# Kernel tuning notes

Measured on AMD Instinct MI355X. Metric: run time of the kernel, lower is better.

Reference implementation:

```python
import jax, jax.numpy as jnp
import numpy as np

B, T, H, L = 64, 256, 512, 2

def setup_inputs() -> dict:
    key = jax.random.key(0)
    ks = jax.random.split(key, 5)
    s = 0.05  # keep gate pre-activations in a sane range
    return {
        "x": jax.random.normal(ks[0], (B, T, H), jnp.float32),
        "Wi": jax.random.normal(ks[1], (L, H, 4 * H), jnp.float32) * s,
        "Wh": jax.random.normal(ks[2], (L, H, 4 * H), jnp.float32) * s,
        "bi": jax.random.normal(ks[3], (L, 4 * H), jnp.float32) * s,
        "bh": jax.random.normal(ks[4], (L, 4 * H), jnp.float32) * s,
    }

def _lstm(x, Wi, Wh, bi, bh):
    b, t, _ = x.shape
    L_, H_ = Wi.shape[0], Wi.shape[2] // 4
    h0 = jnp.zeros((L_, b, H_), x.dtype)
    c0 = jnp.zeros((L_, b, H_), x.dtype)

    def step(carry, x_t):
        h, c = carry
        hs, cs = [], []
        inp = x_t  # [B, H]
        for l in range(L_):
            gates = inp @ Wi[l] + bi[l] + h[l] @ Wh[l] + bh[l]  # [B, 4H]
            i, f, g, o = jnp.split(gates, 4, axis=-1)
            i, f, o = jax.nn.sigmoid(i), jax.nn.sigmoid(f), jax.nn.sigmoid(o)
            g = jnp.tanh(g)
            new_c = f * c[l] + i * g
            new_h = o * jnp.tanh(new_c)
            hs.append(new_h)
            cs.append(new_c)
            inp = new_h
        return (jnp.stack(hs), jnp.stack(cs)), inp

    (hT, cT), outs = jax.lax.scan(step, (h0, c0), jnp.swapaxes(x, 0, 1))
    return jnp.swapaxes(outs, 0, 1), (hT, cT)  # [B,T,H], ([L,B,H],[L,B,H])

def reference(x, Wi, Wh, bi, bh):
    return _lstm(x, Wi, Wh, bi, bh)
```

## Files before the change

kernel.cpp:

```cpp
#include <hip/hip_runtime.h>

typedef __attribute__((ext_vector_type(8))) short short8;
typedef __attribute__((ext_vector_type(4))) float f32x4;
typedef __attribute__((ext_vector_type(4))) float fvec4;
typedef __attribute__((ext_vector_type(4))) unsigned short u16x4;

#define B_ 64
#define T_ 256
#define H_ 512
#define NG 2048
#define BTH (64*256*512)
#define BH (64*512)
#define FPAD 64

__device__ __forceinline__ float bf2f(unsigned short u) {
    return __builtin_bit_cast(float, ((unsigned)u) << 16);
}
__device__ __forceinline__ unsigned short f2bf(float f) {
    unsigned u = __builtin_bit_cast(unsigned, f);
    u += 0x7fffu + ((u >> 16) & 1u);
    return (unsigned short)(u >> 16);
}
__device__ __forceinline__ float sigm(float x) { return 1.f / (1.f + __expf(-x)); }
__device__ __forceinline__ float tanh_f(float x) {
    x = fminf(15.f, fmaxf(-15.f, x));
    float e = __expf(-2.f * x);
    return (1.f - e) / (1.f + e);
}

__device__ __forceinline__ void store_coh(unsigned* p, unsigned v) {
    __hip_atomic_store(p, v, __ATOMIC_RELAXED, __HIP_MEMORY_SCOPE_AGENT);
}
__device__ __forceinline__ void drain_vm() {
    asm volatile("s_waitcnt vmcnt(0)" ::: "memory");
}
__device__ __forceinline__ void wv_wait(const unsigned* fl, int w, unsigned target) {
    const unsigned* p = fl + (size_t)(((threadIdx.x & 31) << 2) + w) * FPAD;
    int spins = 0;
    for (;;) {
        unsigned v = __hip_atomic_load(p, __ATOMIC_RELAXED, __HIP_MEMORY_SCOPE_AGENT);
        if (__all((int)(v >= target))) break;
        __builtin_amdgcn_s_sleep(1);
        if (++spins > 400000) break;
    }
    asm volatile("" ::: "memory");
}

__global__ void transpose_cvt(const float* __restrict__ Wi, const float* __restrict__ Wh,
                              unsigned short* __restrict__ Wt) {
    __shared__ float tile[64][65];
    int z = blockIdx.z;
    const float* src = (z < 2 ? Wi : Wh) + (size_t)(z & 1) * H_ * NG;
    unsigned short* dst = Wt + (size_t)z * NG * H_;
    int k0 = blockIdx.x * 64, n0 = blockIdx.y * 64;
    int tx = threadIdx.x & 63, ty = threadIdx.x >> 6;
#pragma unroll
    for (int p = 0; p < 16; ++p) {
        int r = (p << 2) + ty;
        tile[r][tx] = src[(size_t)(k0 + r) * NG + n0 + tx];
    }
    __syncthreads();
#pragma unroll
    for (int p = 0; p < 16; ++p) {
        int r = (p << 2) + ty;
        dst[(size_t)(n0 + r) * H_ + k0 + tx] = f2bf(tile[tx][r]);
    }
}

__global__ void cvt_bf16(const float* __restrict__ x, unsigned short* __restrict__ xb) {
    size_t i = ((size_t)blockIdx.x * 256 + threadIdx.x) * 4;
    fvec4 v = *(const fvec4*)&x[i];
    u16x4 o;
    o[0] = f2bf(v[0]); o[1] = f2bf(v[1]); o[2] = f2bf(v[2]); o[3] = f2bf(v[3]);
    *(u16x4*)&xb[i] = o;
}

__global__ __launch_bounds__(256) void gemm_bt(
    const unsigned short* __restrict__ A, const unsigned short* __restrict__ Bt,
    const float* __restrict__ bias1, const float* __restrict__ bias2,
    unsigned short* __restrict__ C) {
    const int tid = threadIdx.x;
    const int wave = tid >> 6, lane = tid & 63;
    const int quad = lane >> 4, l15 = lane & 15;
    const int row0 = blockIdx.x * 64 + wave * 16;
    const int col0 = blockIdx.y * 64;
    f32x4 acc[4] = {};
    const unsigned short* ap = A + (size_t)(row0 + l15) * H_ + (quad << 3);
    const unsigned short* bp = Bt + (size_t)(col0 + l15) * H_ + (quad << 3);
#pragma unroll
    for (int kk = 0; kk < H_; kk += 32) {
        short8 a = *(const short8*)(ap + kk);
#pragma unroll
        for (int c4 = 0; c4 < 4; ++c4) {
            short8 b = *(const short8*)(bp + (size_t)(c4 << 4) * H_ + kk);
            acc[c4] = __builtin_amdgcn_mfma_f32_16x16x32_bf16(a, b, acc[c4], 0, 0, 0);
        }
    }
#pragma unroll
    for (int c4 = 0; c4 < 4; ++c4) {
        int col = col0 + (c4 << 4) + l15;
        float bs = bias1[col] + bias2[col];
        int g = col >> 9;
        int blk = (col & 511) >> 4;
#pragma unroll
        for (int r = 0; r < 4; ++r) {
            int row = row0 + (quad << 2) + r;
            int t = row & 255, b = row >> 8;
            C[((size_t)blk << 20) + ((size_t)t << 12) + (g << 10) + (b << 4) + l15] =
                f2bf(acc[c4][r] + bs);
        }
    }
}

__global__ __launch_bounds__(256, 1) void lstm_fused(
    const unsigned short* __restrict__ Gi,
    const unsigned short* __restrict__ Wt,
    unsigned* __restrict__ h0h,
    unsigned* __restrict__ h1h,
    const float* __restrict__ bi, const float* __restrict__ bh,
    float* __restrict__ out,
    float* __restrict__ hT, float* __restrict__ cT,
    unsigned* __restrict__ flags) {
    __shared__ unsigned short wi_lds[64 * 512];
    const size_t NK = (size_t)NG * H_;
    const int tid = threadIdx.x;
    const int wave = tid >> 6, lane = tid & 63;
    const int quad = lane >> 4, l15 = lane & 15;
    const int m0 = wave << 4;
    unsigned* flag0 = flags;
    unsigned* flag1 = flags + 128 * FPAD;
    const size_t hoff = ((size_t)(quad >> 1) << 9) + ((size_t)(m0 + l15) << 3) + ((quad & 1) << 2);

    if (blockIdx.x < 32) {
        const int slot = (int)blockIdx.x;
        const int j0 = slot << 4;
        const unsigned short* Wht = Wt + 2 * NK;
        short8 bw[64];
#pragma unroll
        for (int kb = 0; kb < 16; ++kb)
#pragma unroll
            for (int g = 0; g < 4; ++g)
                bw[kb * 4 + g] =
                    *(const short8*)&Wht[(size_t)((g << 9) + j0 + l15) * H_ + (kb << 5) + (quad << 3)];
#pragma unroll
        for (int i = 0; i < 64; ++i) asm volatile("" : "+v"(bw[i]));

        if (!(l15 & 1)) {
            unsigned* hz = h0h + ((size_t)(slot * 64) << 3) + (l15 >> 1);
#pragma unroll
            for (int r = 0; r < 4; ++r)
                store_coh(&hz[(size_t)(m0 + (quad << 2) + r) << 3], 0u);
        }
        float cc[4] = {0.f, 0.f, 0.f, 0.f};
        drain_vm();
        store_coh(&flag0[(size_t)((slot << 2) + wave) * FPAD], 1u);

        float gv[4][4];
#pragma unroll
        for (int r = 0; r < 4; ++r) {
            int b = m0 + (quad << 2) + r;
#pragma unroll
            for (int g = 0; g < 4; ++g)
                gv[g][r] = bf2f(Gi[((size_t)slot << 20) + (g << 10) + (b << 4) + l15]);
        }

        for (int t = 0; t < T_; ++t) {
            wv_wait(flag0, wave, (unsigned)(t + 1));
            const unsigned* ap = h0h + ((size_t)t << 14) + hoff;
            short8 ha[16];
#pragma unroll
            for (int kb = 0; kb < 16; ++kb) ha[kb] = *(const short8*)(ap + (kb << 10));

            f32x4 acc0 = {}, acc1 = {}, acc2 = {}, acc3 = {};
#pragma unroll
            for (int kb = 0; kb < 16; ++kb) {
                acc0 = __builtin_amdgcn_mfma_f32_16x16x32_bf16(ha[kb], bw[kb * 4 + 0], acc0, 0, 0, 0);
                acc1 = __builtin_amdgcn_mfma_f32_16x16x32_bf16(ha[kb], bw[kb * 4 + 1], acc1, 0, 0, 0);
                acc2 = __builtin_amdgcn_mfma_f32_16x16x32_bf16(ha[kb], bw[kb * 4 + 2], acc2, 0, 0, 0);
                acc3 = __builtin_amdgcn_mfma_f32_16x16x32_bf16(ha[kb], bw[kb * 4 + 3], acc3, 0, 0, 0);
            }

            unsigned* hw = h0h + ((size_t)(t + 1) << 14) + ((size_t)(slot * 64) << 3) + (l15 >> 1);
            float hvv[4];
#pragma unroll
            for (int r = 0; r < 4; ++r) {
                float iv = sigm(acc0[r] + gv[0][r]);
                float fv = sigm(acc1[r] + gv[1][r]);
                float gg = tanh_f(acc2[r] + gv[2][r]);
                float ov = sigm(acc3[r] + gv[3][r]);
                float cn = fv * cc[r] + iv * gg;
                cc[r] = cn;
                float hv = ov * tanh_f(cn);
                hvv[r] = hv;
                unsigned short hb16 = f2bf(hv);
                unsigned packed = (unsigned)hb16 |
                                  (((unsigned)(unsigned short)__shfl_xor((int)hb16, 1)) << 16);
                if (!(l15 & 1))
                    store_coh(&hw[(size_t)(m0 + (quad << 2) + r) << 3], packed);
            }
            if (t == T_ - 1) {
#pragma unroll
                for (int r = 0; r < 4; ++r) {
                    int b = m0 + (quad << 2) + r;
                    int jj = j0 + l15;
                    hT[((size_t)b << 9) + jj] = hvv[r];
                    cT[((size_t)b << 9) + jj] = cc[r];
                }
            }
            drain_vm();
            store_coh(&flag0[(size_t)((slot << 2) + wave) * FPAD], (unsigned)(t + 2));

            int tn = (t + 1) & (T_ - 1);
#pragma unroll
            for (int r = 0; r < 4; ++r) {
                int b = m0 + (quad << 2) + r;
#pragma unroll
                for (int g = 0; g < 4; ++g)
                    gv[g][r] = bf2f(Gi[((size_t)slot << 20) + ((size_t)tn << 12) +
                                       (g << 10) + (b << 4) + l15]);
            }
        }
    } else {
        const int slot = (int)blockIdx.x - 32;
        const int j0 = slot << 4;
        const unsigned short* Wht = Wt + 3 * NK;
        short8 bw[64];
#pragma unroll
        for (int kb = 0; kb < 16; ++kb)
#pragma unroll
            for (int g = 0; g < 4; ++g)
                bw[kb * 4 + g] =
                    *(const short8*)&Wht[(size_t)((g << 9) + j0 + l15) * H_ + (kb << 5) + (quad << 3)];
#pragma unroll
        for (int i = 0; i < 64; ++i) asm volatile("" : "+v"(bw[i]));

        const unsigned short* Wit = Wt + 1 * NK;
#pragma unroll
        for (int i2 = 0; i2 < 16; ++i2) {
            int c = i2 * 256 + tid;
            int l = c & 15, q = (c >> 4) & 3, g = (c >> 6) & 3, kb = c >> 8;
            short8 v = *(const short8*)&Wit[(size_t)((g << 9) + j0 + l) * H_ + (kb << 5) + (q << 3)];
            *(short8*)((char*)wi_lds + ((size_t)c << 4)) = v;
        }
        __syncthreads();
        const int wbase = (quad << 8) + (l15 << 4);

        float gb0 = bi[NG + j0 + l15]        + bh[NG + j0 + l15];
        float gb1 = bi[NG + 512 + j0 + l15]  + bh[NG + 512 + j0 + l15];
        float gb2 = bi[NG + 1024 + j0 + l15] + bh[NG + 1024 + j0 + l15];
        float gb3 = bi[NG + 1536 + j0 + l15] + bh[NG + 1536 + j0 + l15];

        if (!(l15 & 1)) {
            unsigned* hz = h1h + ((size_t)(slot * 64) << 3) + (l15 >> 1);
#pragma unroll
            for (int r = 0; r < 4; ++r)
                store_coh(&hz[(size_t)(m0 + (quad << 2) + r) << 3], 0u);
        }
        float cc[4] = {0.f, 0.f, 0.f, 0.f};
        drain_vm();
        store_coh(&flag1[(size_t)((slot << 2) + wave) * FPAD], 1u);

        short8 ha1[16], ha0[16];
        wv_wait(flag1, wave, 1u);
        {
            const unsigned* ap1 = h1h + hoff;
#pragma unroll
            for (int kb = 0; kb < 16; ++kb) ha1[kb] = *(const short8*)(ap1 + (kb << 10));
        }
        wv_wait(flag0, wave, 2u);
        {
            const unsigned* ap0 = h0h + ((size_t)1 << 14) + hoff;
#pragma unroll
            for (int kb = 0; kb < 16; ++kb) ha0[kb] = *(const short8*)(ap0 + (kb << 10));
        }

        for (int t = 0; t < T_; ++t) {
            f32x4 acc0 = {}, acc1 = {}, acc2 = {}, acc3 = {};
#pragma unroll
            for (int kb = 0; kb < 16; ++kb) {
                acc0 = __builtin_amdgcn_mfma_f32_16x16x32_bf16(ha1[kb], bw[kb * 4 + 0], acc0, 0, 0, 0);
                acc1 = __builtin_amdgcn_mfma_f32_16x16x32_bf16(ha1[kb], bw[kb * 4 + 1], acc1, 0, 0, 0);
                acc2 = __builtin_amdgcn_mfma_f32_16x16x32_bf16(ha1[kb], bw[kb * 4 + 2], acc2, 0, 0, 0);
                acc3 = __builtin_amdgcn_mfma_f32_16x16x32_bf16(ha1[kb], bw[kb * 4 + 3], acc3, 0, 0, 0);
            }
#pragma unroll
            for (int kb = 0; kb < 16; ++kb) {
                const char* base = (const char*)wi_lds + (kb << 12) + wbase;
                short8 w0 = *(const short8*)(base);
                short8 w1 = *(const short8*)(base + (1 << 10));
                short8 w2 = *(const short8*)(base + (2 << 10));
                short8 w3 = *(const short8*)(base + (3 << 10));
                acc0 = __builtin_amdgcn_mfma_f32_16x16x32_bf16(ha0[kb], w0, acc0, 0, 0, 0);
                acc1 = __builtin_amdgcn_mfma_f32_16x16x32_bf16(ha0[kb], w1, acc1, 0, 0, 0);
                acc2 = __builtin_amdgcn_mfma_f32_16x16x32_bf16(ha0[kb], w2, acc2, 0, 0, 0);
                acc3 = __builtin_amdgcn_mfma_f32_16x16x32_bf16(ha0[kb], w3, acc3, 0, 0, 0);
            }

            unsigned* hw = h1h + ((size_t)(t + 1) << 14) + ((size_t)(slot * 64) << 3) + (l15 >> 1);
            float hvv[4];
#pragma unroll
            for (int r = 0; r < 4; ++r) {
                float iv = sigm(acc0[r] + gb0);
                float fv = sigm(acc1[r] + gb1);
                float gg = tanh_f(acc2[r] + gb2);
                float ov = sigm(acc3[r] + gb3);
                float cn = fv * cc[r] + iv * gg;
                cc[r] = cn;
                float hv = ov * tanh_f(cn);
                hvv[r] = hv;
                unsigned short hb16 = f2bf(hv);
                unsigned packed = (unsigned)hb16 |
                                  (((unsigned)(unsigned short)__shfl_xor((int)hb16, 1)) << 16);
                if (!(l15 & 1))
                    store_coh(&hw[(size_t)(m0 + (quad << 2) + r) << 3], packed);
            }
#pragma unroll
            for (int r = 0; r < 4; ++r) {
                int b = m0 + (quad << 2) + r;
                int jj = j0 + l15;
                out[((size_t)((b << 8) + t)) * H_ + jj] = hvv[r];
            }
            if (t == T_ - 1) {
#pragma unroll
                for (int r = 0; r < 4; ++r) {
                    int b = m0 + (quad << 2) + r;
                    int jj = j0 + l15;
                    hT[BH + ((size_t)b << 9) + jj] = hvv[r];
                    cT[BH + ((size_t)b << 9) + jj] = cc[r];
                }
                break;
            }
            drain_vm();
            store_coh(&flag1[(size_t)((slot << 2) + wave) * FPAD], (unsigned)(t + 2));

            wv_wait(flag0, wave, (unsigned)(t + 3));
            const unsigned* ap0 = h0h + ((size_t)(t + 2) << 14) + hoff;
#pragma unroll
            for (int kb = 0; kb < 16; ++kb) ha0[kb] = *(const short8*)(ap0 + (kb << 10));
            wv_wait(flag1, wave, (unsigned)(t + 2));
            const unsigned* ap1 = h1h + ((size_t)(t + 1) << 14) + hoff;
#pragma unroll
            for (int kb = 0; kb < 16; ++kb) ha1[kb] = *(const short8*)(ap1 + (kb << 10));
        }
    }
}

extern "C" void kernel_launch(void* const* d_in, const int* in_sizes, int n_in,
                              void* d_out, int out_size, void* d_ws, size_t ws_size,
                              hipStream_t stream) {
    const float* x  = (const float*)d_in[0];
    const float* Wi = (const float*)d_in[1];
    const float* Wh = (const float*)d_in[2];
    const float* bi = (const float*)d_in[3];
    const float* bh = (const float*)d_in[4];
    float* out = (float*)d_out;

    char* w = (char*)d_ws;
    const size_t NK = (size_t)NG * H_;
    unsigned short* Wt  = (unsigned short*)w;
    unsigned short* xb  = Wt + 4 * NK;
    unsigned short* Gi  = xb + (size_t)16384 * H_;
    unsigned* h0h       = (unsigned*)(Gi + (size_t)16384 * NG);
    unsigned* h1h       = h0h + (size_t)(T_ + 1) * 16384;
    unsigned* flags     = h1h + (size_t)(T_ + 1) * 16384;

    hipMemsetAsync(flags, 0, 2 * 128 * FPAD * sizeof(unsigned), stream);

    transpose_cvt<<<dim3(8, 32, 4), 256, 0, stream>>>(Wi, Wh, Wt);
    cvt_bf16<<<8192, 256, 0, stream>>>(x, xb);

    gemm_bt<<<dim3(256, 32), 256, 0, stream>>>(xb, Wt + 0 * NK, bi, bh, Gi);

    lstm_fused<<<64, 256, 0, stream>>>(Gi, Wt, h0h, h1h, bi, bh,
                                       out, out + BTH, out + BTH + 2 * (size_t)BH, flags);
}
```

Before: 2.137 ms.

## Fuse layer-0 input projection into recurrent kernel and merge layer-1 flag waits

Removes the separate input-projection GEMM and its Gi buffer. Layer-0 blocks now compute x_t·Wi on the fly from LDS-resident Wi, using an x layout transposed to time-major, and prefetch the next timestep's x after publishing h. Layer-1 blocks use one combined spin-wait on both layer flags per step instead of two sequential waits, and no longer prefetch across iterations. This saves the GEMM launch and its memory traffic, but adds MFMA and LDS work to layer 0's serial critical path.

After: 2.966 ms. +38.8%, slower.

```diff
diff --git a/kernel.cpp b/kernel.cpp
--- a/kernel.cpp
+++ b/kernel.cpp
@@ -45,6 +45,21 @@
     }
     asm volatile("" ::: "memory");
 }
+__device__ __forceinline__ void wv_wait2(const unsigned* fA, unsigned tA,
+                                         const unsigned* fB, unsigned tB, int w) {
+    const int l = threadIdx.x & 63;
+    const unsigned* p = (l < 32) ? fA + (size_t)(((l & 31) << 2) + w) * FPAD
+                                 : fB + (size_t)(((l & 31) << 2) + w) * FPAD;
+    const unsigned tgt = (l < 32) ? tA : tB;
+    int spins = 0;
+    for (;;) {
+        unsigned v = __hip_atomic_load(p, __ATOMIC_RELAXED, __HIP_MEMORY_SCOPE_AGENT);
+        if (__all((int)(v >= tgt))) break;
+        __builtin_amdgcn_s_sleep(1);
+        if (++spins > 400000) break;
+    }
+    asm volatile("" ::: "memory");
+}
 
 __global__ void transpose_cvt(const float* __restrict__ Wi, const float* __restrict__ Wh,
                               unsigned short* __restrict__ Wt) {
@@ -67,53 +82,19 @@
     }
 }
 
-__global__ void cvt_bf16(const float* __restrict__ x, unsigned short* __restrict__ xb) {
+__global__ void cvt_blk(const float* __restrict__ x, unsigned short* __restrict__ xb) {
     size_t i = ((size_t)blockIdx.x * 256 + threadIdx.x) * 4;
+    int h = (int)(i & 511);
+    size_t r2 = i >> 9;
+    int t = (int)(r2 & 255), b = (int)(r2 >> 8);
     fvec4 v = *(const fvec4*)&x[i];
     u16x4 o;
     o[0] = f2bf(v[0]); o[1] = f2bf(v[1]); o[2] = f2bf(v[2]); o[3] = f2bf(v[3]);
-    *(u16x4*)&xb[i] = o;
-}
-
-__global__ __launch_bounds__(256) void gemm_bt(
-    const unsigned short* __restrict__ A, const unsigned short* __restrict__ Bt,
-    const float* __restrict__ bias1, const float* __restrict__ bias2,
-    unsigned short* __restrict__ C) {
-    const int tid = threadIdx.x;
-    const int wave = tid >> 6, lane = tid & 63;
-    const int quad = lane >> 4, l15 = lane & 15;
-    const int row0 = blockIdx.x * 64 + wave * 16;
-    const int col0 = blockIdx.y * 64;
-    f32x4 acc[4] = {};
-    const unsigned short* ap = A + (size_t)(row0 + l15) * H_ + (quad << 3);
-    const unsigned short* bp = Bt + (size_t)(col0 + l15) * H_ + (quad << 3);
-#pragma unroll
-    for (int kk = 0; kk < H_; kk += 32) {
-        short8 a = *(const short8*)(ap + kk);
-#pragma unroll
-        for (int c4 = 0; c4 < 4; ++c4) {
-            short8 b = *(const short8*)(bp + (size_t)(c4 << 4) * H_ + kk);
-            acc[c4] = __builtin_amdgcn_mfma_f32_16x16x32_bf16(a, b, acc[c4], 0, 0, 0);
-        }
-    }
-#pragma unroll
-    for (int c4 = 0; c4 < 4; ++c4) {
-        int col = col0 + (c4 << 4) + l15;
-        float bs = bias1[col] + bias2[col];
-        int g = col >> 9;
-        int blk = (col & 511) >> 4;
-#pragma unroll
-        for (int r = 0; r < 4; ++r) {
-            int row = row0 + (quad << 2) + r;
-            int t = row & 255, b = row >> 8;
-            C[((size_t)blk << 20) + ((size_t)t << 12) + (g << 10) + (b << 4) + l15] =
-                f2bf(acc[c4][r] + bs);
-        }
-    }
+    *(u16x4*)&xb[(((size_t)t << 6) + b) * H_ + h] = o;
 }
 
 __global__ __launch_bounds__(256, 1) void lstm_fused(
-    const unsigned short* __restrict__ Gi,
+    const unsigned short* __restrict__ xb,
     const unsigned short* __restrict__ Wt,
     unsigned* __restrict__ h0h,
     unsigned* __restrict__ h1h,
@@ -130,38 +111,55 @@
     unsigned* flag0 = flags;
     unsigned* flag1 = flags + 128 * FPAD;
     const size_t hoff = ((size_t)(quad >> 1) << 9) + ((size_t)(m0 + l15) << 3) + ((quad & 1) << 2);
-
-    if (blockIdx.x < 32) {
-        const int slot = (int)blockIdx.x;
-        const int j0 = slot << 4;
-        const unsigned short* Wht = Wt + 2 * NK;
-        short8 bw[64];
-#pragma unroll
-        for (int kb = 0; kb < 16; ++kb)
-#pragma unroll
-            for (int g = 0; g < 4; ++g)
-                bw[kb * 4 + g] =
-                    *(const short8*)&Wht[(size_t)((g << 9) + j0 + l15) * H_ + (kb << 5) + (quad << 3)];
-#pragma unroll
-        for (int i = 0; i < 64; ++i) asm volatile("" : "+v"(bw[i]));
-
+    const int wbase = (quad << 8) + (l15 << 4);
+    const int is_l1 = (blockIdx.x >= 32);
+    const int slot = (int)blockIdx.x & 31;
+    const int j0 = slot << 4;
+
+    const unsigned short* Wht = Wt + (is_l1 ? 3 : 2) * NK;
+    short8 bw[64];
+#pragma unroll
+    for (int kb = 0; kb < 16; ++kb)
+#pragma unroll
+        for (int g = 0; g < 4; ++g)
+            bw[kb * 4 + g] =
+                *(const short8*)&Wht[(size_t)((g << 9) + j0 + l15) * H_ + (kb << 5) + (quad << 3)];
+#pragma unroll
+    for (int i = 0; i < 64; ++i) asm volatile("" : "+v"(bw[i]));
+
+    const unsigned short* Wit = Wt + (is_l1 ? 1 : 0) * NK;
+#pragma unroll
+    for (int i2 = 0; i2 < 16; ++i2) {
+        int c = i2 * 256 + tid;
+        int l = c & 15, q = (c >> 4) & 3, g = (c >> 6) & 3, kb = c >> 8;
+        short8 v = *(const short8*)&Wit[(size_t)((g << 9) + j0 + l) * H_ + (kb << 5) + (q << 3)];
+        *(short8*)((char*)wi_lds + ((size_t)c << 4)) = v;
+    }
+    __syncthreads();
+
+    const int boff = is_l1 ? NG : 0;
+    float gb0 = bi[boff + j0 + l15]        + bh[boff + j0 + l15];
+    float gb1 = bi[boff + 512 + j0 + l15]  + bh[boff + 512 + j0 + l15];
+    float gb2 = bi[boff + 1024 + j0 + l15] + bh[boff + 1024 + j0 + l15];
+    float gb3 = bi[boff + 1536 + j0 + l15] + bh[boff + 1536 + j0 + l15];
+
+    float cc[4] = {0.f, 0.f, 0.f, 0.f};
+
+    if (!is_l1) {
         if (!(l15 & 1)) {
             unsigned* hz = h0h + ((size_t)(slot * 64) << 3) + (l15 >> 1);
 #pragma unroll
             for (int r = 0; r < 4; ++r)
                 store_coh(&hz[(size_t)(m0 + (quad << 2) + r) << 3], 0u);
         }
-        float cc[4] = {0.f, 0.f, 0.f, 0.f};
         drain_vm();
         store_coh(&flag0[(size_t)((slot << 2) + wave) * FPAD], 1u);
 
-        float gv[4][4];
-#pragma unroll
-        for (int r = 0; r < 4; ++r) {
-            int b = m0 + (quad << 2) + r;
-#pragma unroll
-            for (int g = 0; g < 4; ++g)
-                gv[g][r] = bf2f(Gi[((size_t)slot << 20) + (g << 10) + (b << 4) + l15]);
+        short8 xa[16];
+        {
+            const unsigned short* xp = xb + (size_t)(m0 + l15) * H_ + (quad << 3);
+#pragma unroll
+            for (int kb = 0; kb < 16; ++kb) xa[kb] = *(const short8*)(xp + (kb << 5));
         }
 
         for (int t = 0; t < T_; ++t) {
@@ -178,110 +176,6 @@
                 acc1 = __builtin_amdgcn_mfma_f32_16x16x32_bf16(ha[kb], bw[kb * 4 + 1], acc1, 0, 0, 0);
                 acc2 = __builtin_amdgcn_mfma_f32_16x16x32_bf16(ha[kb], bw[kb * 4 + 2], acc2, 0, 0, 0);
                 acc3 = __builtin_amdgcn_mfma_f32_16x16x32_bf16(ha[kb], bw[kb * 4 + 3], acc3, 0, 0, 0);
-            }
-
-            unsigned* hw = h0h + ((size_t)(t + 1) << 14) + ((size_t)(slot * 64) << 3) + (l15 >> 1);
-            float hvv[4];
-#pragma unroll
-            for (int r = 0; r < 4; ++r) {
-                float iv = sigm(acc0[r] + gv[0][r]);
-                float fv = sigm(acc1[r] + gv[1][r]);
-                float gg = tanh_f(acc2[r] + gv[2][r]);
-                float ov = sigm(acc3[r] + gv[3][r]);
-                float cn = fv * cc[r] + iv * gg;
-                cc[r] = cn;
-                float hv = ov * tanh_f(cn);
-                hvv[r] = hv;
-                unsigned short hb16 = f2bf(hv);
-                unsigned packed = (unsigned)hb16 |
-                                  (((unsigned)(unsigned short)__shfl_xor((int)hb16, 1)) << 16);
-                if (!(l15 & 1))
-                    store_coh(&hw[(size_t)(m0 + (quad << 2) + r) << 3], packed);
-            }
-            if (t == T_ - 1) {
-#pragma unroll
-                for (int r = 0; r < 4; ++r) {
-                    int b = m0 + (quad << 2) + r;
-                    int jj = j0 + l15;
-                    hT[((size_t)b << 9) + jj] = hvv[r];
-                    cT[((size_t)b << 9) + jj] = cc[r];
-                }
-            }
-            drain_vm();
-            store_coh(&flag0[(size_t)((slot << 2) + wave) * FPAD], (unsigned)(t + 2));
-
-            int tn = (t + 1) & (T_ - 1);
-#pragma unroll
-            for (int r = 0; r < 4; ++r) {
-                int b = m0 + (quad << 2) + r;
-#pragma unroll
-                for (int g = 0; g < 4; ++g)
-                    gv[g][r] = bf2f(Gi[((size_t)slot << 20) + ((size_t)tn << 12) +
-                                       (g << 10) + (b << 4) + l15]);
-            }
-        }
-    } else {
-        const int slot = (int)blockIdx.x - 32;
-        const int j0 = slot << 4;
-        const unsigned short* Wht = Wt + 3 * NK;
-        short8 bw[64];
-#pragma unroll
-        for (int kb = 0; kb < 16; ++kb)
-#pragma unroll
-            for (int g = 0; g < 4; ++g)
-                bw[kb * 4 + g] =
-                    *(const short8*)&Wht[(size_t)((g << 9) + j0 + l15) * H_ + (kb << 5) + (quad << 3)];
-#pragma unroll
-        for (int i = 0; i < 64; ++i) asm volatile("" : "+v"(bw[i]));
-
-        const unsigned short* Wit = Wt + 1 * NK;
-#pragma unroll
-        for (int i2 = 0; i2 < 16; ++i2) {
-            int c = i2 * 256 + tid;
-            int l = c & 15, q = (c >> 4) & 3, g = (c >> 6) & 3, kb = c >> 8;
-            short8 v = *(const short8*)&Wit[(size_t)((g << 9) + j0 + l) * H_ + (kb << 5) + (q << 3)];
-            *(short8*)((char*)wi_lds + ((size_t)c << 4)) = v;
-        }
-        __syncthreads();
-        const int wbase = (quad << 8) + (l15 << 4);
-
-        float gb0 = bi[NG + j0 + l15]        + bh[NG + j0 + l15];
-        float gb1 = bi[NG + 512 + j0 + l15]  + bh[NG + 512 + j0 + l15];
-        float gb2 = bi[NG + 1024 + j0 + l15] + bh[NG + 1024 + j0 + l15];
-        float gb3 = bi[NG + 1536 + j0 + l15] + bh[NG + 1536 + j0 + l15];
-
-        if (!(l15 & 1)) {
-            unsigned* hz = h1h + ((size_t)(slot * 64) << 3) + (l15 >> 1);
-#pragma unroll
-            for (int r = 0; r < 4; ++r)
-                store_coh(&hz[(size_t)(m0 + (quad << 2) + r) << 3], 0u);
-        }
-        float cc[4] = {0.f, 0.f, 0.f, 0.f};
-        drain_vm();
-        store_coh(&flag1[(size_t)((slot << 2) + wave) * FPAD], 1u);
-
-        short8 ha1[16], ha0[16];
-        wv_wait(flag1, wave, 1u);
-        {
-            const unsigned* ap1 = h1h + hoff;
-#pragma unroll
-            for (int kb = 0; kb < 16; ++kb) ha1[kb] = *(const short8*)(ap1 + (kb << 10));
-        }
-        wv_wait(flag0, wave, 2u);
-        {
-            const unsigned* ap0 = h0h + ((size_t)1 << 14) + hoff;
-#pragma unroll
-            for (int kb = 0; kb < 16; ++kb) ha0[kb] = *(const short8*)(ap0 + (kb << 10));
-        }
-
-        for (int t = 0; t < T_; ++t) {
-            f32x4 acc0 = {}, acc1 = {}, acc2 = {}, acc3 = {};
-#pragma unroll
-            for (int kb = 0; kb < 16; ++kb) {
-                acc0 = __builtin_amdgcn_mfma_f32_16x16x32_bf16(ha1[kb], bw[kb * 4 + 0], acc0, 0, 0, 0);
-                acc1 = __builtin_amdgcn_mfma_f32_16x16x32_bf16(ha1[kb], bw[kb * 4 + 1], acc1, 0, 0, 0);
-                acc2 = __builtin_amdgcn_mfma_f32_16x16x32_bf16(ha1[kb], bw[kb * 4 + 2], acc2, 0, 0, 0);
-                acc3 = __builtin_amdgcn_mfma_f32_16x16x32_bf16(ha1[kb], bw[kb * 4 + 3], acc3, 0, 0, 0);
             }
 #pragma unroll
             for (int kb = 0; kb < 16; ++kb) {
@@ -290,13 +184,13 @@
                 short8 w1 = *(const short8*)(base + (1 << 10));
                 short8 w2 = *(const short8*)(base + (2 << 10));
                 short8 w3 = *(const short8*)(base + (3 << 10));
-                acc0 = __builtin_amdgcn_mfma_f32_16x16x32_bf16(ha0[kb], w0, acc0, 0, 0, 0);
-                acc1 = __builtin_amdgcn_mfma_f32_16x16x32_bf16(ha0[kb], w1, acc1, 0, 0, 0);
-                acc2 = __builtin_amdgcn_mfma_f32_16x16x32_bf16(ha0[kb], w2, acc2, 0, 0, 0);
-                acc3 = __builtin_amdgcn_mfma_f32_16x16x32_bf16(ha0[kb], w3, acc3, 0, 0, 0);
-            }
-
-            unsigned* hw = h1h + ((size_t)(t + 1) << 14) + ((size_t)(slot * 64) << 3) + (l15 >> 1);
+                acc0 = __builtin_amdgcn_mfma_f32_16x16x32_bf16(xa[kb], w0, acc0, 0, 0, 0);
+                acc1 = __builtin_amdgcn_mfma_f32_16x16x32_bf16(xa[kb], w1, acc1, 0, 0, 0);
+                acc2 = __builtin_amdgcn_mfma_f32_16x16x32_bf16(xa[kb], w2, acc2, 0, 0, 0);
+                acc3 = __builtin_amdgcn_mfma_f32_16x16x32_bf16(xa[kb], w3, acc3, 0, 0, 0);
+            }
+
+            unsigned* hw = h0h + ((size_t)(t + 1) << 14) + ((size_t)(slot * 64) << 3) + (l15 >> 1);
             float hvv[4];
 #pragma unroll
             for (int r = 0; r < 4; ++r) {
@@ -314,6 +208,86 @@
                 if (!(l15 & 1))
                     store_coh(&hw[(size_t)(m0 + (quad << 2) + r) << 3], packed);
             }
+            drain_vm();
+            store_coh(&flag0[(size_t)((slot << 2) + wave) * FPAD], (unsigned)(t + 2));
+
+            if (t < T_ - 1) {
+                const unsigned short* xp =
+                    xb + (((size_t)(t + 1) << 6) + (m0 + l15)) * H_ + (quad << 3);
+#pragma unroll
+                for (int kb = 0; kb < 16; ++kb) xa[kb] = *(const short8*)(xp + (kb << 5));
+            } else {
+#pragma unroll
+                for (int r = 0; r < 4; ++r) {
+                    int b = m0 + (quad << 2) + r;
+                    int jj = j0 + l15;
+                    hT[((size_t)b << 9) + jj] = hvv[r];
+                    cT[((size_t)b << 9) + jj] = cc[r];
+                }
+            }
+        }
+    } else {
+        if (!(l15 & 1)) {
+            unsigned* hz = h1h + ((size_t)(slot * 64) << 3) + (l15 >> 1);
+#pragma unroll
+            for (int r = 0; r < 4; ++r)
+                store_coh(&hz[(size_t)(m0 + (quad << 2) + r) << 3], 0u);
+        }
+        drain_vm();
+        store_coh(&flag1[(size_t)((slot << 2) + wave) * FPAD], 1u);
+
+        for (int t = 0; t < T_; ++t) {
+            wv_wait2(flag1, (unsigned)(t + 1), flag0, (unsigned)(t + 2), wave);
+            const unsigned* ap1 = h1h + ((size_t)t << 14) + hoff;
+            const unsigned* ap0 = h0h + ((size_t)(t + 1) << 14) + hoff;
+            short8 ha1[16], ha0[16];
+#pragma unroll
+            for (int kb = 0; kb < 16; ++kb) ha1[kb] = *(const short8*)(ap1 + (kb << 10));
+#pragma unroll
+            for (int kb = 0; kb < 16; ++kb) ha0[kb] = *(const short8*)(ap0 + (kb << 10));
+
+            f32x4 acc0 = {}, acc1 = {}, acc2 = {}, acc3 = {};
+#pragma unroll
+            for (int kb = 0; kb < 16; ++kb) {
+                acc0 = __builtin_amdgcn_mfma_f32_16x16x32_bf16(ha1[kb], bw[kb * 4 + 0], acc0, 0, 0, 0);
+                acc1 = __builtin_amdgcn_mfma_f32_16x16x32_bf16(ha1[kb], bw[kb * 4 + 1], acc1, 0, 0, 0);
+                acc2 = __builtin_amdgcn_mfma_f32_16x16x32_bf16(ha1[kb], bw[kb * 4 + 2], acc2, 0, 0, 0);
+                acc3 = __builtin_amdgcn_mfma_f32_16x16x32_bf16(ha1[kb], bw[kb * 4 + 3], acc3, 0, 0, 0);
+            }
+#pragma unroll
+            for (int kb = 0; kb < 16; ++kb) {
+                const char* base = (const char*)wi_lds + (kb << 12) + wbase;
+                short8 w0 = *(const short8*)(base);
+                short8 w1 = *(const short8*)(base + (1 << 10));
+                short8 w2 = *(const short8*)(base + (2 << 10));
+                short8 w3 = *(const short8*)(base + (3 << 10));
+                acc0 = __builtin_amdgcn_mfma_f32_16x16x32_bf16(ha0[kb], w0, acc0, 0, 0, 0);
+                acc1 = __builtin_amdgcn_mfma_f32_16x16x32_bf16(ha0[kb], w1, acc1, 0, 0, 0);
+                acc2 = __builtin_amdgcn_mfma_f32_16x16x32_bf16(ha0[kb], w2, acc2, 0, 0, 0);
+                acc3 = __builtin_amdgcn_mfma_f32_16x16x32_bf16(ha0[kb], w3, acc3, 0, 0, 0);
+            }
+
+            unsigned* hw = h1h + ((size_t)(t + 1) << 14) + ((size_t)(slot * 64) << 3) + (l15 >> 1);
+            float hvv[4];
+#pragma unroll
+            for (int r = 0; r < 4; ++r) {
+                float iv = sigm(acc0[r] + gb0);
+                float fv = sigm(acc1[r] + gb1);
+                float gg = tanh_f(acc2[r] + gb2);
+                float ov = sigm(acc3[r] + gb3);
+                float cn = fv * cc[r] + iv * gg;
+                cc[r] = cn;
+                float hv = ov * tanh_f(cn);
+                hvv[r] = hv;
+                unsigned short hb16 = f2bf(hv);
+                unsigned packed = (unsigned)hb16 |
+                                  (((unsigned)(unsigned short)__shfl_xor((int)hb16, 1)) << 16);
+                if (!(l15 & 1))
+                    store_coh(&hw[(size_t)(m0 + (quad << 2) + r) << 3], packed);
+            }
+            drain_vm();
+            store_coh(&flag1[(size_t)((slot << 2) + wave) * FPAD], (unsigned)(t + 2));
+
 #pragma unroll
             for (int r = 0; r < 4; ++r) {
                 int b = m0 + (quad << 2) + r;
@@ -328,19 +302,7 @@
                     hT[BH + ((size_t)b << 9) + jj] = hvv[r];
                     cT[BH + ((size_t)b << 9) + jj] = cc[r];
                 }
-                break;
-            }
-            drain_vm();
-            store_coh(&flag1[(size_t)((slot << 2) + wave) * FPAD], (unsigned)(t + 2));
-
-            wv_wait(flag0, wave, (unsigned)(t + 3));
-            const unsigned* ap0 = h0h + ((size_t)(t + 2) << 14) + hoff;
-#pragma unroll
-            for (int kb = 0; kb < 16; ++kb) ha0[kb] = *(const short8*)(ap0 + (kb << 10));
-            wv_wait(flag1, wave, (unsigned)(t + 2));
-            const unsigned* ap1 = h1h + ((size_t)(t + 1) << 14) + hoff;
-#pragma unroll
-            for (int kb = 0; kb < 16; ++kb) ha1[kb] = *(const short8*)(ap1 + (kb << 10));
+            }
         }
     }
 }
@@ -359,18 +321,15 @@
     const size_t NK = (size_t)NG * H_;
     unsigned short* Wt  = (unsigned short*)w;
     unsigned short* xb  = Wt + 4 * NK;
-    unsigned short* Gi  = xb + (size_t)16384 * H_;
-    unsigned* h0h       = (unsigned*)(Gi + (size_t)16384 * NG);
+    unsigned* h0h       = (unsigned*)(xb + (size_t)16384 * H_);
     unsigned* h1h       = h0h + (size_t)(T_ + 1) * 16384;
     unsigned* flags     = h1h + (size_t)(T_ + 1) * 16384;
 
     hipMemsetAsync(flags, 0, 2 * 128 * FPAD * sizeof(unsigned), stream);
 
     transpose_cvt<<<dim3(8, 32, 4), 256, 0, stream>>>(Wi, Wh, Wt);
-    cvt_bf16<<<8192, 256, 0, stream>>>(x, xb);
-
-    gemm_bt<<<dim3(256, 32), 256, 0, stream>>>(xb, Wt + 0 * NK, bi, bh, Gi);
-
-    lstm_fused<<<64, 256, 0, stream>>>(Gi, Wt, h0h, h1h, bi, bh,
+    cvt_blk<<<8192, 256, 0, stream>>>(x, xb);
+
+    lstm_fused<<<64, 256, 0, stream>>>(xb, Wt, h0h, h1h, bi, bh,
                                        out, out + BTH, out + BTH + 2 * (size_t)BH, flags);
 }
```

## Merge both LSTM layers into one block per slot with a single flag round

Applied to the files above, without the earlier changes.

Replaces the 64-block layout, where 32 blocks ran layer 0 and 32 ran layer 1 with separate flag arrays, with 32 blocks that each compute layer 0 at step rnd and layer 1 at step rnd-1 in the same round. Layer-1 recurrent weights stay in registers, while layer-0 recurrent weights and layer-1 input weights move to two LDS buffers. The aim is one cross-block barrier per round instead of two interleaved dependency chains, halving the number of flags to poll. In exchange each block does twice the MFMA work per step, reads Wh0 from LDS instead of registers, and runs on half as many CUs.

Result: slower. 2.466 ms (+15.4%).

```diff
diff --git a/kernel.cpp b/kernel.cpp
--- a/kernel.cpp
+++ b/kernel.cpp
@@ -121,226 +121,196 @@
     float* __restrict__ out,
     float* __restrict__ hT, float* __restrict__ cT,
     unsigned* __restrict__ flags) {
-    __shared__ unsigned short wi_lds[64 * 512];
+    __shared__ unsigned short w_lds[2][64 * 512];
     const size_t NK = (size_t)NG * H_;
     const int tid = threadIdx.x;
     const int wave = tid >> 6, lane = tid & 63;
     const int quad = lane >> 4, l15 = lane & 15;
     const int m0 = wave << 4;
-    unsigned* flag0 = flags;
-    unsigned* flag1 = flags + 128 * FPAD;
+    const int slot = (int)blockIdx.x;
+    const int j0 = slot << 4;
     const size_t hoff = ((size_t)(quad >> 1) << 9) + ((size_t)(m0 + l15) << 3) + ((quad & 1) << 2);
-
-    if (blockIdx.x < 32) {
-        const int slot = (int)blockIdx.x;
-        const int j0 = slot << 4;
-        const unsigned short* Wht = Wt + 2 * NK;
-        short8 bw[64];
-#pragma unroll
-        for (int kb = 0; kb < 16; ++kb)
-#pragma unroll
-            for (int g = 0; g < 4; ++g)
-                bw[kb * 4 + g] =
-                    *(const short8*)&Wht[(size_t)((g << 9) + j0 + l15) * H_ + (kb << 5) + (quad << 3)];
-#pragma unroll
-        for (int i = 0; i < 64; ++i) asm volatile("" : "+v"(bw[i]));
-
-        if (!(l15 & 1)) {
-            unsigned* hz = h0h + ((size_t)(slot * 64) << 3) + (l15 >> 1);
-#pragma unroll
-            for (int r = 0; r < 4; ++r)
-                store_coh(&hz[(size_t)(m0 + (quad << 2) + r) << 3], 0u);
-        }
-        float cc[4] = {0.f, 0.f, 0.f, 0.f};
-        drain_vm();
-        store_coh(&flag0[(size_t)((slot << 2) + wave) * FPAD], 1u);
-
-        float gv[4][4];
-#pragma unroll
-        for (int r = 0; r < 4; ++r) {
-            int b = m0 + (quad << 2) + r;
-#pragma unroll
-            for (int g = 0; g < 4; ++g)
-                gv[g][r] = bf2f(Gi[((size_t)slot << 20) + (g << 10) + (b << 4) + l15]);
-        }
-
-        for (int t = 0; t < T_; ++t) {
-            wv_wait(flag0, wave, (unsigned)(t + 1));
-            const unsigned* ap = h0h + ((size_t)t << 14) + hoff;
-            short8 ha[16];
-#pragma unroll
-            for (int kb = 0; kb < 16; ++kb) ha[kb] = *(const short8*)(ap + (kb << 10));
-
-            f32x4 acc0 = {}, acc1 = {}, acc2 = {}, acc3 = {};
+    const int wbase = (quad << 8) + (l15 << 4);
+
+    const unsigned short* Wh1t = Wt + 3 * NK;
+    short8 bw[64];
+#pragma unroll
+    for (int kb = 0; kb < 16; ++kb)
+#pragma unroll
+        for (int g = 0; g < 4; ++g)
+            bw[kb * 4 + g] =
+                *(const short8*)&Wh1t[(size_t)((g << 9) + j0 + l15) * H_ + (kb << 5) + (quad << 3)];
+#pragma unroll
+    for (int i = 0; i < 64; ++i) asm volatile("" : "+v"(bw[i]));
+
+    {
+        const unsigned short* srcs[2] = {Wt + 2 * NK, Wt + 1 * NK};
+#pragma unroll
+        for (int i2 = 0; i2 < 32; ++i2) {
+            int c = i2 * 256 + tid;
+            int sl = c >> 12, cc_ = c & 4095;
+            int l = cc_ & 15, q = (cc_ >> 4) & 3, g = (cc_ >> 6) & 3, kb = cc_ >> 8;
+            short8 v = *(const short8*)&srcs[sl][(size_t)((g << 9) + j0 + l) * H_ +
+                                                 (kb << 5) + (q << 3)];
+            *(short8*)((char*)&w_lds[sl][0] + ((size_t)cc_ << 4)) = v;
+        }
+    }
+
+    store_coh(&h0h[(size_t)slot * 512 + tid], 0u);
+    store_coh(&h0h[(size_t)slot * 512 + 256 + tid], 0u);
+    store_coh(&h1h[(size_t)slot * 512 + tid], 0u);
+    store_coh(&h1h[(size_t)slot * 512 + 256 + tid], 0u);
+    __syncthreads();
+    if (lane == 0) store_coh(&flags[(size_t)((slot << 2) + wave) * FPAD], 1u);
+
+    float gb0 = bi[NG + j0 + l15]        + bh[NG + j0 + l15];
+    float gb1 = bi[NG + 512 + j0 + l15]  + bh[NG + 512 + j0 + l15];
+    float gb2 = bi[NG + 1024 + j0 + l15] + bh[NG + 1024 + j0 + l15];
+    float gb3 = bi[NG + 1536 + j0 + l15] + bh[NG + 1536 + j0 + l15];
+
+    float gv[4][4];
+#pragma unroll
+    for (int r = 0; r < 4; ++r) {
+        int b = m0 + (quad << 2) + r;
+#pragma unroll
+        for (int g = 0; g < 4; ++g)
+            gv[g][r] = bf2f(Gi[((size_t)slot << 20) + (g << 10) + (b << 4) + l15]);
+    }
+
+    float cc0[4] = {0.f, 0.f, 0.f, 0.f};
+    float cc1[4] = {0.f, 0.f, 0.f, 0.f};
+
+    for (int rnd = 0; rnd <= T_; ++rnd) {
+        wv_wait(flags, wave, (unsigned)(rnd + 1));
+
+        const unsigned* ap0 = h0h + ((size_t)rnd << 14) + hoff;
+        short8 ha0[16];
+#pragma unroll
+        for (int kb = 0; kb < 16; ++kb) ha0[kb] = *(const short8*)(ap0 + (kb << 10));
+        short8 ha1[16];
+        if (rnd > 0) {
+            const unsigned* ap1 = h1h + ((size_t)(rnd - 1) << 14) + hoff;
+#pragma unroll
+            for (int kb = 0; kb < 16; ++kb) ha1[kb] = *(const short8*)(ap1 + (kb << 10));
+        }
+
+        if (rnd < T_) {
+            f32x4 a0 = {}, a1 = {}, a2 = {}, a3 = {};
 #pragma unroll
             for (int kb = 0; kb < 16; ++kb) {
-                acc0 = __builtin_amdgcn_mfma_f32_16x16x32_bf16(ha[kb], bw[kb * 4 + 0], acc0, 0, 0, 0);
-                acc1 = __builtin_amdgcn_mfma_f32_16x16x32_bf16(ha[kb], bw[kb * 4 + 1], acc1, 0, 0, 0);
-                acc2 = __builtin_amdgcn_mfma_f32_16x16x32_bf16(ha[kb], bw[kb * 4 + 2], acc2, 0, 0, 0);
-                acc3 = __builtin_amdgcn_mfma_f32_16x16x32_bf16(ha[kb], bw[kb * 4 + 3], acc3, 0, 0, 0);
-            }
-
-            unsigned* hw = h0h + ((size_t)(t + 1) << 14) + ((size_t)(slot * 64) << 3) + (l15 >> 1);
+                const char* base = (const char*)&w_lds[0][0] + (kb << 12) + wbase;
+                short8 w0 = *(const short8*)(base);
+                short8 w1 = *(const short8*)(base + (1 << 10));
+                short8 w2 = *(const short8*)(base + (2 << 10));
+                short8 w3 = *(const short8*)(base + (3 << 10));
+                a0 = __builtin_amdgcn_mfma_f32_16x16x32_bf16(ha0[kb], w0, a0, 0, 0, 0);
+                a1 = __builtin_amdgcn_mfma_f32_16x16x32_bf16(ha0[kb], w1, a1, 0, 0, 0);
+                a2 = __builtin_amdgcn_mfma_f32_16x16x32_bf16(ha0[kb], w2, a2, 0, 0, 0);
+                a3 = __builtin_amdgcn_mfma_f32_16x16x32_bf16(ha0[kb], w3, a3, 0, 0, 0);
+            }
+            unsigned* hw0 = h0h + ((size_t)(rnd + 1) << 14) + ((size_t)(slot * 64) << 3) + (l15 >> 1);
             float hvv[4];
 #pragma unroll
             for (int r = 0; r < 4; ++r) {
-                float iv = sigm(acc0[r] + gv[0][r]);
-                float fv = sigm(acc1[r] + gv[1][r]);
-                float gg = tanh_f(acc2[r] + gv[2][r]);
-                float ov = sigm(acc3[r] + gv[3][r]);
-                float cn = fv * cc[r] + iv * gg;
-                cc[r] = cn;
+                float iv = sigm(a0[r] + gv[0][r]);
+                float fv = sigm(a1[r] + gv[1][r]);
+                float gg = tanh_f(a2[r] + gv[2][r]);
+                float ov = sigm(a3[r] + gv[3][r]);
+                float cn = fv * cc0[r] + iv * gg;
+                cc0[r] = cn;
                 float hv = ov * tanh_f(cn);
                 hvv[r] = hv;
                 unsigned short hb16 = f2bf(hv);
                 unsigned packed = (unsigned)hb16 |
                                   (((unsigned)(unsigned short)__shfl_xor((int)hb16, 1)) << 16);
                 if (!(l15 & 1))
-                    store_coh(&hw[(size_t)(m0 + (quad << 2) + r) << 3], packed);
-            }
-            if (t == T_ - 1) {
+                    store_coh(&hw0[(size_t)(m0 + (quad << 2) + r) << 3], packed);
+            }
+            if (rnd == T_ - 1) {
 #pragma unroll
                 for (int r = 0; r < 4; ++r) {
                     int b = m0 + (quad << 2) + r;
                     int jj = j0 + l15;
                     hT[((size_t)b << 9) + jj] = hvv[r];
-                    cT[((size_t)b << 9) + jj] = cc[r];
+                    cT[((size_t)b << 9) + jj] = cc0[r];
                 }
             }
-            drain_vm();
-            store_coh(&flag0[(size_t)((slot << 2) + wave) * FPAD], (unsigned)(t + 2));
-
-            int tn = (t + 1) & (T_ - 1);
-#pragma unroll
-            for (int r = 0; r < 4; ++r) {
-                int b = m0 + (quad << 2) + r;
-#pragma unroll
-                for (int g = 0; g < 4; ++g)
-                    gv[g][r] = bf2f(Gi[((size_t)slot << 20) + ((size_t)tn << 12) +
-                                       (g << 10) + (b << 4) + l15]);
-            }
-        }
-    } else {
-        const int slot = (int)blockIdx.x - 32;
-        const int j0 = slot << 4;
-        const unsigned short* Wht = Wt + 3 * NK;
-        short8 bw[64];
-#pragma unroll
-        for (int kb = 0; kb < 16; ++kb)
-#pragma unroll
-            for (int g = 0; g < 4; ++g)
-                bw[kb * 4 + g] =
-                    *(const short8*)&Wht[(size_t)((g << 9) + j0 + l15) * H_ + (kb << 5) + (quad << 3)];
-#pragma unroll
-        for (int i = 0; i < 64; ++i) asm volatile("" : "+v"(bw[i]));
-
-        const unsigned short* Wit = Wt + 1 * NK;
-#pragma unroll
-        for (int i2 = 0; i2 < 16; ++i2) {
-            int c = i2 * 256 + tid;
-            int l = c & 15, q = (c >> 4) & 3, g = (c >> 6) & 3, kb = c >> 8;
-            short8 v = *(const short8*)&Wit[(size_t)((g << 9) + j0 + l) * H_ + (kb << 5) + (q << 3)];
-            *(short8*)((char*)wi_lds + ((size_t)c << 4)) = v;
-        }
-        __syncthreads();
-        const int wbase = (quad << 8) + (l15 << 4);
-
-        float gb0 = bi[NG + j0 + l15]        + bh[NG + j0 + l15];
-        float gb1 = bi[NG + 512 + j0 + l15]  + bh[NG + 512 + j0 + l15];
-        float gb2 = bi[NG + 1024 + j0 + l15] + bh[NG + 1024 + j0 + l15];
-        float gb3 = bi[NG + 1536 + j0 + l15] + bh[NG + 1536 + j0 + l15];
-
-        if (!(l15 & 1)) {
-            unsigned* hz = h1h + ((size_t)(slot * 64) << 3) + (l15 >> 1);
-#pragma unroll
-            for (int r = 0; r < 4; ++r)
-                store_coh(&hz[(size_t)(m0 + (quad << 2) + r) << 3], 0u);
-        }
-        float cc[4] = {0.f, 0.f, 0.f, 0.f};
-        drain_vm();
-        store_coh(&flag1[(size_t)((slot << 2) + wave) * FPAD], 1u);
-
-        short8 ha1[16], ha0[16];
-        wv_wait(flag1, wave, 1u);
-        {
-            const unsigned* ap1 = h1h + hoff;
-#pragma unroll
-            for (int kb = 0; kb < 16; ++kb) ha1[kb] = *(const short8*)(ap1 + (kb << 10));
-        }
-        wv_wait(flag0, wave, 2u);
-        {
-            const unsigned* ap0 = h0h + ((size_t)1 << 14) + hoff;
-#pragma unroll
-            for (int kb = 0; kb < 16; ++kb) ha0[kb] = *(const short8*)(ap0 + (kb << 10));
-        }
-
-        for (int t = 0; t < T_; ++t) {
-            f32x4 acc0 = {}, acc1 = {}, acc2 = {}, acc3 = {};
+        }
+
+        float hv1[4];
+        if (rnd > 0) {
+            f32x4 a0 = {}, a1 = {}, a2 = {}, a3 = {};
 #pragma unroll
             for (int kb = 0; kb < 16; ++kb) {
-                acc0 = __builtin_amdgcn_mfma_f32_16x16x32_bf16(ha1[kb], bw[kb * 4 + 0], acc0, 0, 0, 0);
-                acc1 = __builtin_amdgcn_mfma_f32_16x16x32_bf16(ha1[kb], bw[kb * 4 + 1], acc1, 0, 0, 0);
-                acc2 = __builtin_amdgcn_mfma_f32_16x16x32_bf16(ha1[kb], bw[kb * 4 + 2], acc2, 0, 0, 0);
-                acc3 = __builtin_amdgcn_mfma_f32_16x16x32_bf16(ha1[kb], bw[kb * 4 + 3], acc3, 0, 0, 0);
+                a0 = __builtin_amdgcn_mfma_f32_16x16x32_bf16(ha1[kb], bw[kb * 4 + 0], a0, 0, 0, 0);
+                a1 = __builtin_amdgcn_mfma_f32_16x16x32_bf16(ha1[kb], bw[kb * 4 + 1], a1, 0, 0, 0);
+                a2 = __builtin_amdgcn_mfma_f32_16x16x32_bf16(ha1[kb], bw[kb * 4 + 2], a2, 0, 0, 0);
+                a3 = __builtin_amdgcn_mfma_f32_16x16x32_bf16(ha1[kb], bw[kb * 4 + 3], a3, 0, 0, 0);
             }
 #pragma unroll
             for (int kb = 0; kb < 16; ++kb) {
-                const char* base = (const char*)wi_lds + (kb << 12) + wbase;
+                const char* base = (const char*)&w_lds[1][0] + (kb << 12) + wbase;
                 short8 w0 = *(const short8*)(base);
                 short8 w1 = *(const short8*)(base + (1 << 10));
                 short8 w2 = *(const short8*)(base + (2 << 10));
                 short8 w3 = *(const short8*)(base + (3 << 10));
-                acc0 = __builtin_amdgcn_mfma_f32_16x16x32_bf16(ha0[kb], w0, acc0, 0, 0, 0);
-                acc1 = __builtin_amdgcn_mfma_f32_16x16x32_bf16(ha0[kb], w1, acc1, 0, 0, 0);
-                acc2 = __builtin_amdgcn_mfma_f32_16x16x32_bf16(ha0[kb], w2, acc2, 0, 0, 0);
-                acc3 = __builtin_amdgcn_mfma_f32_16x16x32_bf16(ha0[kb], w3, acc3, 0, 0, 0);
-            }
-
-            unsigned* hw = h1h + ((size_t)(t + 1) << 14) + ((size_t)(slot * 64) << 3) + (l15 >> 1);
-            float hvv[4];
+                a0 = __builtin_amdgcn_mfma_f32_16x16x32_bf16(ha0[kb], w0, a0, 0, 0, 0);
+                a1 = __builtin_amdgcn_mfma_f32_16x16x32_bf16(ha0[kb], w1, a1, 0, 0, 0);
+                a2 = __builtin_amdgcn_mfma_f32_16x16x32_bf16(ha0[kb], w2, a2, 0, 0, 0);
+                a3 = __builtin_amdgcn_mfma_f32_16x16x32_bf16(ha0[kb], w3, a3, 0, 0, 0);
+            }
+            unsigned* hw1 = h1h + ((size_t)rnd << 14) + ((size_t)(slot * 64) << 3) + (l15 >> 1);
 #pragma unroll
             for (int r = 0; r < 4; ++r) {
-                float iv = sigm(acc0[r] + gb0);
-                float fv = sigm(acc1[r] + gb1);
-                float gg = tanh_f(acc2[r] + gb2);
-                float ov = sigm(acc3[r] + gb3);
-                float cn = fv * cc[r] + iv * gg;
-                cc[r] = cn;
+                float iv = sigm(a0[r] + gb0);
+                float fv = sigm(a1[r] + gb1);
+                float gg = tanh_f(a2[r] + gb2);
+                float ov = sigm(a3[r] + gb3);
+                float cn = fv * cc1[r] + iv * gg;
+                cc1[r] = cn;
                 float hv = ov * tanh_f(cn);
-                hvv[r] = hv;
+                hv1[r] = hv;
                 unsigned short hb16 = f2bf(hv);
                 unsigned packed = (unsigned)hb16 |
                                   (((unsigned)(unsigned short)__shfl_xor((int)hb16, 1)) << 16);
                 if (!(l15 & 1))
-                    store_coh(&hw[(size_t)(m0 + (quad << 2) + r) << 3], packed);
-            }
+                    store_coh(&hw1[(size_t)(m0 + (quad << 2) + r) << 3], packed);
+            }
+        }
+
+        if (rnd < T_) {
+            drain_vm();
+            if (lane == 0) store_coh(&flags[(size_t)((slot << 2) + wave) * FPAD],
+                                     (unsigned)(rnd + 2));
+        }
+
+        if (rnd > 0) {
+            int t1 = rnd - 1;
 #pragma unroll
             for (int r = 0; r < 4; ++r) {
                 int b = m0 + (quad << 2) + r;
                 int jj = j0 + l15;
-                out[((size_t)((b << 8) + t)) * H_ + jj] = hvv[r];
-            }
-            if (t == T_ - 1) {
+                out[((size_t)((b << 8) + t1)) * H_ + jj] = hv1[r];
+            }
+            if (rnd == T_) {
 #pragma unroll
                 for (int r = 0; r < 4; ++r) {
                     int b = m0 + (quad << 2) + r;
                     int jj = j0 + l15;
-                    hT[BH + ((size_t)b << 9) + jj] = hvv[r];
-                    cT[BH + ((size_t)b << 9) + jj] = cc[r];
+                    hT[BH + ((size_t)b << 9) + jj] = hv1[r];
+                    cT[BH + ((size_t)b << 9) + jj] = cc1[r];
                 }
-                break;
-            }
-            drain_vm();
-            store_coh(&flag1[(size_t)((slot << 2) + wave) * FPAD], (unsigned)(t + 2));
-
-            wv_wait(flag0, wave, (unsigned)(t + 3));
-            const unsigned* ap0 = h0h + ((size_t)(t + 2) << 14) + hoff;
-#pragma unroll
-            for (int kb = 0; kb < 16; ++kb) ha0[kb] = *(const short8*)(ap0 + (kb << 10));
-            wv_wait(flag1, wave, (unsigned)(t + 2));
-            const unsigned* ap1 = h1h + ((size_t)(t + 1) << 14) + hoff;
-#pragma unroll
-            for (int kb = 0; kb < 16; ++kb) ha1[kb] = *(const short8*)(ap1 + (kb << 10));
+            }
+        }
+        if (rnd + 1 < T_) {
+#pragma unroll
+            for (int r = 0; r < 4; ++r) {
+                int b = m0 + (quad << 2) + r;
+#pragma unroll
+                for (int g = 0; g < 4; ++g)
+                    gv[g][r] = bf2f(Gi[((size_t)slot << 20) + ((size_t)(rnd + 1) << 12) +
+                                       (g << 10) + (b << 4) + l15]);
+            }
         }
     }
 }
@@ -364,13 +334,13 @@
     unsigned* h1h       = h0h + (size_t)(T_ + 1) * 16384;
     unsigned* flags     = h1h + (size_t)(T_ + 1) * 16384;
 
-    hipMemsetAsync(flags, 0, 2 * 128 * FPAD * sizeof(unsigned), stream);
+    hipMemsetAsync(flags, 0, 128 * FPAD * sizeof(unsigned), stream);
 
     transpose_cvt<<<dim3(8, 32, 4), 256, 0, stream>>>(Wi, Wh, Wt);
     cvt_bf16<<<8192, 256, 0, stream>>>(x, xb);
 
     gemm_bt<<<dim3(256, 32), 256, 0, stream>>>(xb, Wt + 0 * NK, bi, bh, Gi);
 
-    lstm_fused<<<64, 256, 0, stream>>>(Gi, Wt, h0h, h1h, bi, bh,
+    lstm_fused<<<32, 256, 0, stream>>>(Gi, Wt, h0h, h1h, bi, bh,
                                        out, out + BTH, out + BTH + 2 * (size_t)BH, flags);
 }
```
